# Kernel optimization log

Measured on AMD Instinct MI355X. Metric: run time of the kernel, lower is better.

Reference implementation:

```python
import jax, jax.numpy as jnp
import numpy as np

N = 10000      # nodes
ND = 64        # node_dim
H = 128        # hidden_dim
L = 4          # num_layers
K = 16         # knn k
TD = 16        # time_dim


def _time_embed(t, n):
    # sinusoidal embedding, matches _time_embed: freqs = exp(linspace(0,1,half)*-4)
    half = TD // 2
    freqs = jnp.exp(jnp.linspace(0.0, 1.0, half) * -4.0)            # [half]
    angles = t.reshape(1, 1) * freqs[None, :]                        # [1, half]
    emb = jnp.concatenate([jnp.sin(angles), jnp.cos(angles)], -1)    # [1, TD]
    return jnp.broadcast_to(emb, (n, TD))


def _knn_edges(pos, k):
    # full cdist + topk, mirroring _knn_graph (no_grad in torch)
    n = pos.shape[0]
    sq = jnp.sum(pos * pos, -1)
    d2 = sq[:, None] + sq[None, :] - 2.0 * (pos @ pos.T)             # [N, N]
    idxr = jnp.arange(n)
    d2 = d2.at[idxr, idxr].set(jnp.inf)
    _, nbr = jax.lax.top_k(-d2, k)                                   # [N, K] nearest
    src = jnp.repeat(idxr, k)
    dst = nbr.reshape(-1)
    return src, dst


def _egnn_layer(h, pos, src, dst, s, ew1, eb1, ew2, eb2, nw1, nb1, nw2, nb2, cw, cb):
    n = h.shape[0]
    diff = pos[dst] - pos[src]                                       # [E, 3]
    r2 = jnp.sum(diff * diff, -1, keepdims=True)                     # [E, 1]
    r = jnp.sqrt(r2 + 1e-8)
    dir_ij = diff / r
    e_in = jnp.concatenate([h[dst], h[src], r2], -1)                 # [E, 2H+1]
    m = jax.nn.silu(e_in @ ew1 + eb1)
    m = jax.nn.silu(m @ ew2 + eb2)                                   # [E, H]
    m = m * s[src][:, None]                                          # s-gate
    m_sum = jax.ops.segment_sum(m, dst, num_segments=n)              # [N, H]
    deg = jax.ops.segment_sum(jnp.ones((m.shape[0], 1), m.dtype), dst, num_segments=n)
    deg = jnp.maximum(deg, 1.0)
    m_sum = m_sum / deg
    hn = jax.nn.silu(jnp.concatenate([h, m_sum], -1) @ nw1 + nb1)
    h_new = hn @ nw2 + nb2                                           # [N, H]
    gamma = m @ cw + cb                                              # [E, 1]
    cu = jax.ops.segment_sum(gamma * dir_ij, dst, num_segments=n) / deg
    return h_new, pos + cu


def setup_inputs() -> dict:
    key = jax.random.key(0)
    ks = jax.random.split(key, 24)
    g = lambda k, shape: (jax.random.normal(k, shape, dtype=jnp.float32) * 0.05)
    z = lambda shape: jnp.zeros(shape, jnp.float32)
    return {
        'x': jax.random.normal(ks[0], (N, ND), jnp.float32),
        'pos': jax.random.normal(ks[1], (N, 3), jnp.float32) * 5.0,
        't': jax.random.uniform(ks[2], (1,), jnp.float32),
        's': jax.random.uniform(ks[3], (N,), jnp.float32),
        'proj_w': g(ks[4], (ND + 1 + TD, H)), 'proj_b': z((H,)),
        'edge_w1': g(ks[5], (L, 2 * H + 1, H)), 'edge_b1': z((L, H)),
        'edge_w2': g(ks[6], (L, H, H)), 'edge_b2': z((L, H)),
        'node_w1': g(ks[7], (L, 2 * H, H)), 'node_b1': z((L, H)),
        'node_w2': g(ks[8], (L, H, H)), 'node_b2': z((L, H)),
        'coord_w': g(ks[9], (L, H, 1)), 'coord_b': z((L, 1)),
        'ec_w': g(ks[10], (H, 3)), 'ec_b': z((3,)),
        'ef_w': g(ks[11], (H, ND)), 'ef_b': z((ND,)),
    }


def reference(x, pos, t, s, proj_w, proj_b, edge_w1, edge_b1, edge_w2, edge_b2,
              node_w1, node_b1, node_w2, node_b2, coord_w, coord_b,
              ec_w, ec_b, ef_w, ef_b):
    n = x.shape[0]
    src, dst = _knn_edges(jax.lax.stop_gradient(pos), K)  # graph build is no_grad
    temb = _time_embed(t[0], n)
    h = jnp.concatenate([x, s[:, None], temb], -1) @ proj_w + proj_b  # [N, H]
    p = pos
    for l in range(L):
        h, p = _egnn_layer(h, p, src, dst, s,
                           edge_w1[l], edge_b1[l], edge_w2[l], edge_b2[l],
                           node_w1[l], node_b1[l], node_w2[l], node_b2[l],
                           coord_w[l], coord_b[l])
    eps_c = h @ ec_w + ec_b                                           # [N, 3]
    eps_f = h @ ef_w + ef_b                                           # [N, ND]
    return jnp.concatenate([eps_c, eps_f, p], -1)                     # [N, 3+ND+3]
```

## Files before the change

### kernel.cpp

```cpp
#include <hip/hip_runtime.h>
#include <math.h>

#define N_NODES 10000
#define ND 64
#define H 128
#define LAYERS 4
#define KNN 16
#define TD 16
#define E_EDGES (N_NODES * KNN)
#define KC 1250
#define TILE_E 128
#define INF __builtin_inff()

typedef __attribute__((ext_vector_type(8))) short short8;
typedef __attribute__((ext_vector_type(4))) float f32x4;

__device__ __forceinline__ float silu(float x) {
  return x * __builtin_amdgcn_rcpf(1.0f + __expf(-x));
}

__device__ __forceinline__ unsigned short f2bf(float f) {
  unsigned int u = __float_as_uint(f);
  u += 0x7fffu + ((u >> 16) & 1u);
  return (unsigned short)(u >> 16);
}
__device__ __forceinline__ float bf2f(unsigned short h) {
  return __uint_as_float(((unsigned int)h) << 16);
}

__device__ __forceinline__ float dpp_shr1_f(float x) {
  return __int_as_float(__builtin_amdgcn_update_dpp(
      0, __float_as_int(x), 0x111, 0xF, 0xF, true));
}
__device__ __forceinline__ int dpp_shr1_i(int x) {
  return __builtin_amdgcn_update_dpp(0, x, 0x111, 0xF, 0xF, true);
}
__device__ __forceinline__ float rdlane_f(float x, int sl) {
  return __int_as_float(__builtin_amdgcn_readlane(__float_as_int(x), sl));
}

__global__ __launch_bounds__(256) void init_kernel(
    const float* __restrict__ ew2, const float* __restrict__ nw1,
    const float* __restrict__ nw2, const float* __restrict__ ew1,
    const float* __restrict__ pw, const float* __restrict__ ecw,
    const float* __restrict__ efw, unsigned short* __restrict__ w2T,
    unsigned short* __restrict__ nw1T, unsigned short* __restrict__ nw2T,
    unsigned short* __restrict__ ew1T, unsigned short* __restrict__ pwT,
    unsigned short* __restrict__ owT, const float* __restrict__ pos,
    float4* __restrict__ pos4, float* __restrict__ p0,
    int* __restrict__ degi) {
  int bid = blockIdx.x;
  if (bid < 1624) {
    int i = bid * 256 + threadIdx.x;
    if (i < 65536) {
      int l = i >> 14, rem = i & 16383, c = rem >> 7, o = rem & 127;
      w2T[l * 16384 + o * 128 + c] = f2bf(ew2[i]);
    } else if (i < 196608) {
      int j = i - 65536;
      int l = j >> 15, rem = j & 32767, c2 = rem >> 7, o = rem & 127;
      nw1T[l * 32768 + o * 256 + c2] = f2bf(nw1[j]);
    } else if (i < 262144) {
      int j = i - 196608;
      int l = j >> 14, rem = j & 16383, c = rem >> 7, o = rem & 127;
      nw2T[l * 16384 + o * 128 + c] = f2bf(nw2[j]);
    } else if (i < 393216) {
      int j = i - 262144;
      int l = j >> 15, rem = j & 32767, r = rem >> 7, o = rem & 127;
      int o2 = o + ((r >> 7) << 7);
      int c = r & 127;
      ew1T[l * 32768 + o2 * 128 + c] = f2bf(ew1[l * 257 * 128 + r * 128 + o]);
    } else if (i < 405504) {
      int j = i - 393216;
      int o = j / 96, c = j - o * 96;
      pwT[j] = (c < 81) ? f2bf(pw[c * 128 + o]) : 0;
    } else if (i < 415744) {
      int j = i - 405504;
      int o = j >> 7, c = j & 127;
      float v = 0.0f;
      if (o < 3) v = ecw[c * 3 + o];
      else if (o < 67) v = efw[c * 64 + (o - 3)];
      owT[j] = f2bf(v);
    }
  } else {
    int i = (bid - 1624) * 256 + threadIdx.x;
    if (i >= N_NODES) return;
    float x = pos[i * 3 + 0], y = pos[i * 3 + 1], z = pos[i * 3 + 2];
    pos4[i] = make_float4(x, y, z, x * x + y * y + z * z);
    p0[i * 3 + 0] = x;
    p0[i * 3 + 1] = y;
    p0[i * 3 + 2] = z;
    degi[i] = 0;
  }
}

#define DIST1(pp, d)                                                         \
  d = fmaf(ax, (pp).x, fmaf(ay, (pp).y, fmaf(az, (pp).z, (pp).w)));

#define GRP(dv, gbase)                                                       \
  {                                                                          \
    unsigned long long m = __ballot((dv) < th);                              \
    if (m) {                                                                 \
      while (m) {                                                            \
        int sl = __ffsll((long long)m) - 1;                                  \
        m &= m - 1;                                                          \
        float db = rdlane_f((dv), sl);                                       \
        int gj = (gbase) + sl;                                               \
        float pv = dpp_shr1_f(v);                                            \
        int pid = dpp_shr1_i(id);                                            \
        bool stay = (v <= db);                                               \
        bool tk = (lane == 0) || (pv <= db);                                 \
        v = stay ? v : (tk ? db : pv);                                       \
        id = stay ? id : (tk ? gj : pid);                                    \
      }                                                                      \
      th = rdlane_f(v, 15);                                                  \
    }                                                                        \
  }

#define SELF_FIX(j0base)                                                     \
  {                                                                          \
    unsigned rel = (unsigned)(q - (j0base));                                 \
    if (rel < 256u) {                                                        \
      int rl = (int)(rel & 63u);                                             \
      if (rel < 64u) { if (lane == rl) dA = INF; }                           \
      else if (rel < 128u) { if (lane == rl) dB = INF; }                     \
      else if (rel < 192u) { if (lane == rl) dC = INF; }                     \
      else { if (lane == rl) dD = INF; }                                     \
    }                                                                        \
  }

__global__ __launch_bounds__(256) void knn_kernel(const float4* __restrict__ pos4,
                                                  int* __restrict__ nbr,
                                                  int* __restrict__ degi) {
  __shared__ float4 C[KC];
  int tid = threadIdx.x;
  int lane = tid & 63;
  int wid = tid >> 6;
  int q = blockIdx.x * 4 + wid;
  float4 qp = pos4[q];
  float ax = -2.0f * qp.x, ay = -2.0f * qp.y, az = -2.0f * qp.z;
  float v = INF;
  int id = 0;
  float th = INF;
  for (int base = 0; base < N_NODES; base += KC) {
    __syncthreads();
    for (int jj = tid; jj < KC; jj += 256) C[jj] = pos4[base + jj];
    __syncthreads();
    for (int j0 = 0; j0 < 1024; j0 += 256) {
      float4 pA = C[j0 + lane], pB = C[j0 + 64 + lane];
      float4 pC = C[j0 + 128 + lane], pD = C[j0 + 192 + lane];
      float dA, dB, dC, dD;
      DIST1(pA, dA);
      DIST1(pB, dB);
      DIST1(pC, dC);
      DIST1(pD, dD);
      float mn = fminf(fminf(dA, dB), fminf(dC, dD));
      if (__ballot(mn < th)) {
        int gb = base + j0;
        SELF_FIX(gb);
        GRP(dA, gb);
        GRP(dB, gb + 64);
        GRP(dC, gb + 128);
        GRP(dD, gb + 192);
      }
    }
    {
      float4 pA = C[1024 + lane], pB = C[1088 + lane], pC = C[1152 + lane];
      float dA, dB, dC;
      float dD = INF;
      DIST1(pA, dA);
      DIST1(pB, dB);
      DIST1(pC, dC);
      if (lane < 34) {
        float4 pD = C[1216 + lane];
        DIST1(pD, dD);
      }
      float mn = fminf(fminf(dA, dB), fminf(dC, dD));
      if (__ballot(mn < th)) {
        int gb = base + 1024;
        SELF_FIX(gb);
        GRP(dA, gb);
        GRP(dB, gb + 64);
        GRP(dC, gb + 128);
        GRP(dD, gb + 192);
      }
    }
  }
  if (lane < KNN) {
    nbr[q * KNN + lane] = id;
    atomicAdd(&degi[id], 1);
  }
}

__global__ __launch_bounds__(1024) void scan_kernel(const int* __restrict__ degi,
                                                    int* __restrict__ off,
                                                    int* __restrict__ cursor) {
  __shared__ int part[1024];
  int t = threadIdx.x;
  int base = t * 10;
  int sum = 0;
  if (t < 1000)
    for (int i = 0; i < 10; ++i) sum += degi[base + i];
  part[t] = sum;
  __syncthreads();
  for (int stp = 1; stp < 1024; stp <<= 1) {
    int v = (t >= stp) ? part[t - stp] : 0;
    __syncthreads();
    part[t] += v;
    __syncthreads();
  }
  if (t < 1000) {
    int run = (t == 0) ? 0 : part[t - 1];
    for (int i = 0; i < 10; ++i) {
      off[base + i] = run;
      cursor[base + i] = run;
      run += degi[base + i];
    }
  }
  if (t == 0) off[N_NODES] = E_EDGES;
}

__global__ void scatter_kernel(const int* __restrict__ nbr, int* __restrict__ cursor,
                               int* __restrict__ eid, int* __restrict__ dstof) {
  int e = blockIdx.x * 256 + threadIdx.x;
  if (e < E_EDGES) {
    int d = nbr[e];
    int p = atomicAdd(&cursor[d], 1);
    eid[p] = e;
    dstof[p] = d;
  }
}

__global__ __launch_bounds__(256) void sort_proj_kernel(
    const float* __restrict__ x, const float* __restrict__ s,
    const float* __restrict__ tptr, const unsigned short* __restrict__ pwT,
    const float* __restrict__ pb, const unsigned short* __restrict__ ew1T,
    const float* __restrict__ eb1, float* __restrict__ h_out,
    unsigned short* __restrict__ Abf, unsigned short* __restrict__ Bbf,
    const int* __restrict__ off, int* __restrict__ eid) {
  __shared__ unsigned short inpb[16][104];
  __shared__ unsigned short hb[16][136];
  int tid = threadIdx.x;
  int bid = blockIdx.x;
  if (bid >= 625) {
    int n = (bid - 625) * 256 + tid;
    if (n >= N_NODES) return;
    int a = off[n], b = off[n + 1];
    for (int i = a + 1; i < b; ++i) {
      int v = eid[i];
      int j = i - 1;
      while (j >= a && eid[j] > v) { eid[j + 1] = eid[j]; --j; }
      eid[j + 1] = v;
    }
    return;
  }
  int n0 = bid * 16;
  float t = tptr[0];
  for (int idx = tid; idx < 16 * 104; idx += 256) {
    int n = idx / 104, c = idx - n * 104;
    int gn = n0 + n;
    float val;
    if (c < 64) val = x[gn * ND + c];
    else if (c == 64) val = s[gn];
    else if (c < 81) {
      int j = c - 65;
      int jj = (j < 8) ? j : (j - 8);
      float f = __expf(-4.0f * (float)jj / 7.0f);
      float a = t * f;
      val = (j < 8) ? sinf(a) : cosf(a);
    } else val = 0.0f;
    inpb[n][c] = f2bf(val);
  }
  __syncthreads();
  int w = tid >> 6, lane = tid & 63, fr = lane & 15, kg = lane >> 4;
  f32x4 acc[2];
  acc[0] = (f32x4){0.f, 0.f, 0.f, 0.f};
  acc[1] = (f32x4){0.f, 0.f, 0.f, 0.f};
#pragma unroll
  for (int ks = 0; ks < 3; ++ks) {
    int k = ks * 32 + kg * 8;
    short8 a = *(const short8*)&inpb[fr][k];
#pragma unroll
    for (int nt = 0; nt < 2; ++nt) {
      int col = w * 32 + nt * 16 + fr;
      short8 b = *(const short8*)&pwT[col * 96 + k];
      acc[nt] = __builtin_amdgcn_mfma_f32_16x16x32_bf16(a, b, acc[nt], 0, 0, 0);
    }
  }
#pragma unroll
  for (int nt = 0; nt < 2; ++nt) {
    int col = w * 32 + nt * 16 + fr;
    float bias = pb[col];
#pragma unroll
    for (int r = 0; r < 4; ++r) {
      int row = kg * 4 + r;
      float hv = acc[nt][r] + bias;
      h_out[(n0 + row) * H + col] = hv;
      hb[row][col] = f2bf(hv);
    }
  }
  __syncthreads();
  f32x4 acc2[4];
#pragma unroll
  for (int nt = 0; nt < 4; ++nt) acc2[nt] = (f32x4){0.f, 0.f, 0.f, 0.f};
#pragma unroll
  for (int ks = 0; ks < 4; ++ks) {
    int k = ks * 32 + kg * 8;
    short8 a = *(const short8*)&hb[fr][k];
#pragma unroll
    for (int nt = 0; nt < 4; ++nt) {
      int col = w * 64 + nt * 16 + fr;
      short8 b = *(const short8*)&ew1T[col * H + k];
      acc2[nt] = __builtin_amdgcn_mfma_f32_16x16x32_bf16(a, b, acc2[nt], 0, 0, 0);
    }
  }
#pragma unroll
  for (int nt = 0; nt < 4; ++nt) {
    int col = w * 64 + nt * 16 + fr;
    float bias = (col < H) ? eb1[col] : 0.0f;
#pragma unroll
    for (int r = 0; r < 4; ++r) {
      int row = kg * 4 + r;
      float val = acc2[nt][r] + bias;
      if (col < H) Abf[(n0 + row) * H + col] = f2bf(val);
      else Bbf[(n0 + row) * H + (col - H)] = f2bf(val);
    }
  }
}

__global__ __launch_bounds__(256) void edge_mfma_kernel(
    const unsigned short* __restrict__ Abf, const unsigned short* __restrict__ Bbf,
    const float* __restrict__ p, const float* __restrict__ s,
    const int* __restrict__ csr_off, const int* __restrict__ eid,
    const int* __restrict__ dstof, const float* __restrict__ wr,
    const unsigned short* __restrict__ w2T, const float* __restrict__ eb2,
    const float* __restrict__ cw, const float* __restrict__ cbp,
    float* __restrict__ msA, float* __restrict__ msB,
    float* __restrict__ cuA, float* __restrict__ cuB) {
  __shared__ unsigned short t1s[TILE_E][136];
  __shared__ float r2A[TILE_E], sA[TILE_E], dirA[TILE_E][3], gA[TILE_E];
  __shared__ int srcA[TILE_E], dstA[TILE_E];
  __shared__ float wrs[H], b2s[H], cws[H];

  int tid = threadIdx.x;
  int P0 = blockIdx.x * TILE_E;
  int P1 = P0 + TILE_E;

  if (tid < H) { wrs[tid] = wr[tid]; b2s[tid] = eb2[tid]; cws[tid] = cw[tid]; }
  if (tid < TILE_E) {
    int e = tid;
    int edge = eid[P0 + e];
    int src = edge >> 4;
    int d = dstof[P0 + e];
    srcA[e] = src;
    dstA[e] = d;
    float dx = p[d * 3 + 0] - p[src * 3 + 0];
    float dy = p[d * 3 + 1] - p[src * 3 + 1];
    float dz = p[d * 3 + 2] - p[src * 3 + 2];
    float r2 = dx * dx + dy * dy + dz * dz;
    r2A[e] = r2;
    float rinv = 1.0f / sqrtf(r2 + 1e-8f);
    dirA[e][0] = dx * rinv;
    dirA[e][1] = dy * rinv;
    dirA[e][2] = dz * rinv;
    sA[e] = s[src];
  }
  __syncthreads();

  int nA = dstA[0], nB = dstA[TILE_E - 1];
  int nn = nB - nA + 1;

  for (int idx = tid; idx < TILE_E * 16; idx += 256) {
    int e = idx >> 4, cp = (idx & 15) * 8;
    uint4 au = *(const uint4*)&Abf[dstA[e] * H + cp];
    uint4 bu = *(const uint4*)&Bbf[srcA[e] * H + cp];
    float r2v = r2A[e];
    unsigned int as[4] = {au.x, au.y, au.z, au.w};
    unsigned int bs[4] = {bu.x, bu.y, bu.z, bu.w};
    unsigned int res[4];
#pragma unroll
    for (int q = 0; q < 4; ++q) {
      float pr0 = silu(bf2f((unsigned short)(as[q] & 0xffffu)) +
                       bf2f((unsigned short)(bs[q] & 0xffffu)) +
                       r2v * wrs[cp + 2 * q]);
      float pr1 = silu(bf2f((unsigned short)(as[q] >> 16)) +
                       bf2f((unsigned short)(bs[q] >> 16)) +
                       r2v * wrs[cp + 2 * q + 1]);
      res[q] = ((unsigned int)f2bf(pr1) << 16) | (unsigned int)f2bf(pr0);
    }
    *(uint4*)&t1s[e][cp] = make_uint4(res[0], res[1], res[2], res[3]);
  }
  __syncthreads();

  int w = tid >> 6, lane = tid & 63;
  int fr = lane & 15, kg = lane >> 4;
  f32x4 acc[8][2];
#pragma unroll
  for (int mt = 0; mt < 8; ++mt)
#pragma unroll
    for (int nt = 0; nt < 2; ++nt) acc[mt][nt] = (f32x4){0.f, 0.f, 0.f, 0.f};
#pragma unroll
  for (int ks = 0; ks < 4; ++ks) {
    int k = ks * 32 + kg * 8;
    short8 bf0 = *(const short8*)&w2T[(w * 32 + fr) * H + k];
    short8 bf1 = *(const short8*)&w2T[(w * 32 + 16 + fr) * H + k];
#pragma unroll
    for (int mt = 0; mt < 8; ++mt) {
      short8 a = *(const short8*)&t1s[mt * 16 + fr][k];
      acc[mt][0] = __builtin_amdgcn_mfma_f32_16x16x32_bf16(a, bf0, acc[mt][0], 0, 0, 0);
      acc[mt][1] = __builtin_amdgcn_mfma_f32_16x16x32_bf16(a, bf1, acc[mt][1], 0, 0, 0);
    }
  }
  __syncthreads();

#pragma unroll
  for (int mt = 0; mt < 8; ++mt) {
#pragma unroll
    for (int nt = 0; nt < 2; ++nt) {
      int col = w * 32 + nt * 16 + fr;
      float b2v = b2s[col];
#pragma unroll
      for (int r = 0; r < 4; ++r) {
        int row = mt * 16 + kg * 4 + r;
        float mv = silu(acc[mt][nt][r] + b2v) * sA[row];
        t1s[row][col] = f2bf(mv);
      }
    }
  }
  __syncthreads();

  if (tid < TILE_E) {
    float g = 0.f;
    for (int c = 0; c < H; c += 4) {
      uint2 u = *(const uint2*)&t1s[tid][c];
      g = fmaf(bf2f((unsigned short)(u.x & 0xffffu)), cws[c], g);
      g = fmaf(bf2f((unsigned short)(u.x >> 16)), cws[c + 1], g);
      g = fmaf(bf2f((unsigned short)(u.y & 0xffffu)), cws[c + 2], g);
      g = fmaf(bf2f((unsigned short)(u.y >> 16)), cws[c + 3], g);
    }
    gA[tid] = g + cbp[0];
  }
  __syncthreads();

  for (int idx = tid; idx < nn * 32; idx += 256) {
    int ni = idx >> 5, cq = (idx & 31) * 4;
    int n = nA + ni;
    int o0 = csr_off[n], o1 = csr_off[n + 1];
    int lo = max(o0, P0), hi = min(o1, P1);
    float s0 = 0.f, s1 = 0.f, s2 = 0.f, s3 = 0.f;
    for (int pos = lo; pos < hi; ++pos) {
      uint2 u = *(const uint2*)&t1s[pos - P0][cq];
      s0 += bf2f((unsigned short)(u.x & 0xffffu));
      s1 += bf2f((unsigned short)(u.x >> 16));
      s2 += bf2f((unsigned short)(u.y & 0xffffu));
      s3 += bf2f((unsigned short)(u.y >> 16));
    }
    float4 sv = make_float4(s0, s1, s2, s3);
    if (o0 >= P0) {
      *(float4*)&msA[n * H + cq] = sv;
      if (o1 <= P1) *(float4*)&msB[n * H + cq] = make_float4(0.f, 0.f, 0.f, 0.f);
    } else {
      *(float4*)&msB[n * H + cq] = sv;
    }
  }
  for (int idx = tid; idx < nn * 3; idx += 256) {
    int ni = idx / 3, comp = idx - ni * 3;
    int n = nA + ni;
    int o0 = csr_off[n], o1 = csr_off[n + 1];
    int lo = max(o0, P0), hi = min(o1, P1);
    float sum = 0.f;
    for (int pos = lo; pos < hi; ++pos)
      sum += gA[pos - P0] * dirA[pos - P0][comp];
    if (o0 >= P0) {
      cuA[n * 3 + comp] = sum;
      if (o1 <= P1) cuB[n * 3 + comp] = 0.0f;
    } else {
      cuB[n * 3 + comp] = sum;
    }
  }
}

__global__ __launch_bounds__(256) void node_mfma_kernel(
    const float* __restrict__ h, const float* __restrict__ msA,
    const float* __restrict__ msB, const int* __restrict__ degi,
    const float* __restrict__ cuA, const float* __restrict__ cuB,
    const float* __restrict__ p_in, const unsigned short* __restrict__ w1T,
    const float* __restrict__ nb1, const unsigned short* __restrict__ w2T,
    const float* __restrict__ nb2, const unsigned short* __restrict__ ew1Tn,
    const float* __restrict__ eb1n, int doab, float* __restrict__ h_out,
    float* __restrict__ p_out, unsigned short* __restrict__ Abf,
    unsigned short* __restrict__ Bbf) {
  __shared__ unsigned short insb[16][264];
  __shared__ unsigned short hnsb[16][136];
  int tid = threadIdx.x;
  int n0 = blockIdx.x * 16;
  for (int idx = tid; idx < 16 * 32; idx += 256) {
    int n = idx >> 5, cq = (idx & 31) * 4;
    int gn = n0 + n;
    float4 hv = *(const float4*)&h[gn * H + cq];
    int dg = degi[gn];
    float m0 = 0.f, m1 = 0.f, m2 = 0.f, m3 = 0.f;
    if (dg > 0) {
      float4 a = *(const float4*)&msA[gn * H + cq];
      float4 b = *(const float4*)&msB[gn * H + cq];
      float fdg = (float)dg;
      m0 = (a.x + b.x) / fdg;
      m1 = (a.y + b.y) / fdg;
      m2 = (a.z + b.z) / fdg;
      m3 = (a.w + b.w) / fdg;
    }
    uint2 uh, um;
    uh.x = ((unsigned int)f2bf(hv.y) << 16) | (unsigned int)f2bf(hv.x);
    uh.y = ((unsigned int)f2bf(hv.w) << 16) | (unsigned int)f2bf(hv.z);
    um.x = ((unsigned int)f2bf(m1) << 16) | (unsigned int)f2bf(m0);
    um.y = ((unsigned int)f2bf(m3) << 16) | (unsigned int)f2bf(m2);
    *(uint2*)&insb[n][cq] = uh;
    *(uint2*)&insb[n][H + cq] = um;
  }
  __syncthreads();
  int w = tid >> 6, lane = tid & 63, fr = lane & 15, kg = lane >> 4;
  f32x4 acc[2];
  acc[0] = (f32x4){0.f, 0.f, 0.f, 0.f};
  acc[1] = (f32x4){0.f, 0.f, 0.f, 0.f};
#pragma unroll
  for (int ks = 0; ks < 8; ++ks) {
    int k = ks * 32 + kg * 8;
    short8 a = *(const short8*)&insb[fr][k];
#pragma unroll
    for (int nt = 0; nt < 2; ++nt) {
      int col = w * 32 + nt * 16 + fr;
      short8 b = *(const short8*)&w1T[col * 256 + k];
      acc[nt] = __builtin_amdgcn_mfma_f32_16x16x32_bf16(a, b, acc[nt], 0, 0, 0);
    }
  }
#pragma unroll
  for (int nt = 0; nt < 2; ++nt) {
    int col = w * 32 + nt * 16 + fr;
    float b1 = nb1[col];
#pragma unroll
    for (int r = 0; r < 4; ++r) {
      int row = kg * 4 + r;
      hnsb[row][col] = f2bf(silu(acc[nt][r] + b1));
    }
  }
  __syncthreads();
  f32x4 acc2[2];
  acc2[0] = (f32x4){0.f, 0.f, 0.f, 0.f};
  acc2[1] = (f32x4){0.f, 0.f, 0.f, 0.f};
#pragma unroll
  for (int ks = 0; ks < 4; ++ks) {
    int k = ks * 32 + kg * 8;
    short8 a = *(const short8*)&hnsb[fr][k];
#pragma unroll
    for (int nt = 0; nt < 2; ++nt) {
      int col = w * 32 + nt * 16 + fr;
      short8 b = *(const short8*)&w2T[col * H + k];
      acc2[nt] = __builtin_amdgcn_mfma_f32_16x16x32_bf16(a, b, acc2[nt], 0, 0, 0);
    }
  }
  unsigned short (*hb)[136] = (unsigned short(*)[136])insb;
#pragma unroll
  for (int nt = 0; nt < 2; ++nt) {
    int col = w * 32 + nt * 16 + fr;
    float b2 = nb2[col];
#pragma unroll
    for (int r = 0; r < 4; ++r) {
      int row = kg * 4 + r;
      float hv = acc2[nt][r] + b2;
      h_out[(n0 + row) * H + col] = hv;
      hb[row][col] = f2bf(hv);
    }
  }
  if (tid < 48) {
    int nl = tid / 3, comp = tid - nl * 3;
    int gn = n0 + nl;
    int dg = degi[gn];
    float add = 0.0f;
    if (dg > 0)
      add = (cuA[gn * 3 + comp] + cuB[gn * 3 + comp]) / (float)dg;
    p_out[gn * 3 + comp] = p_in[gn * 3 + comp] + add;
  }
  if (doab) {
    __syncthreads();
    f32x4 acc3[4];
#pragma unroll
    for (int nt = 0; nt < 4; ++nt) acc3[nt] = (f32x4){0.f, 0.f, 0.f, 0.f};
#pragma unroll
    for (int ks = 0; ks < 4; ++ks) {
      int k = ks * 32 + kg * 8;
      short8 a = *(const short8*)&hb[fr][k];
#pragma unroll
      for (int nt = 0; nt < 4; ++nt) {
        int col = w * 64 + nt * 16 + fr;
        short8 b = *(const short8*)&ew1Tn[col * H + k];
        acc3[nt] = __builtin_amdgcn_mfma_f32_16x16x32_bf16(a, b, acc3[nt], 0, 0, 0);
      }
    }
#pragma unroll
    for (int nt = 0; nt < 4; ++nt) {
      int col = w * 64 + nt * 16 + fr;
      float bias = (col < H) ? eb1n[col] : 0.0f;
#pragma unroll
      for (int r = 0; r < 4; ++r) {
        int row = kg * 4 + r;
        float val = acc3[nt][r] + bias;
        if (col < H) Abf[(n0 + row) * H + col] = f2bf(val);
        else Bbf[(n0 + row) * H + (col - H)] = f2bf(val);
      }
    }
  }
}

__global__ __launch_bounds__(256) void out_mfma_kernel(
    const float* __restrict__ h, const float* __restrict__ p,
    const unsigned short* __restrict__ owT, const float* __restrict__ ecb,
    const float* __restrict__ efb, float* __restrict__ out) {
  __shared__ unsigned short hb[16][136];
  int tid = threadIdx.x;
  int n0 = blockIdx.x * 16;
  for (int idx = tid; idx < 16 * H; idx += 256) {
    int n = idx >> 7, c = idx & 127;
    hb[n][c] = f2bf(h[(n0 + n) * H + c]);
  }
  __syncthreads();
  int w = tid >> 6, lane = tid & 63, fr = lane & 15, kg = lane >> 4;
  int ntiles = (w == 0) ? 2 : 1;
  for (int tt = 0; tt < ntiles; ++tt) {
    int tile = (tt == 0) ? w : 4;
    f32x4 acc = (f32x4){0.f, 0.f, 0.f, 0.f};
    int col = tile * 16 + fr;
#pragma unroll
    for (int ks = 0; ks < 4; ++ks) {
      int k = ks * 32 + kg * 8;
      short8 a = *(const short8*)&hb[fr][k];
      short8 b = *(const short8*)&owT[col * H + k];
      acc = __builtin_amdgcn_mfma_f32_16x16x32_bf16(a, b, acc, 0, 0, 0);
    }
    if (col < 67) {
      float bias = (col < 3) ? ecb[col] : efb[col - 3];
#pragma unroll
      for (int r = 0; r < 4; ++r) {
        int row = kg * 4 + r;
        out[(n0 + row) * 70 + col] = acc[r] + bias;
      }
    }
  }
  if (tid < 48) {
    int nl = tid / 3, comp = tid - nl * 3;
    int gn = n0 + nl;
    out[gn * 70 + 67 + comp] = p[gn * 3 + comp];
  }
}

extern "C" void kernel_launch(void* const* d_in, const int* in_sizes, int n_in,
                              void* d_out, int out_size, void* d_ws, size_t ws_size,
                              hipStream_t stream) {
  const float* x = (const float*)d_in[0];
  const float* pos = (const float*)d_in[1];
  const float* t = (const float*)d_in[2];
  const float* s = (const float*)d_in[3];
  const float* pw = (const float*)d_in[4];
  const float* pb = (const float*)d_in[5];
  const float* ew1 = (const float*)d_in[6];
  const float* eb1 = (const float*)d_in[7];
  const float* ew2 = (const float*)d_in[8];
  const float* eb2 = (const float*)d_in[9];
  const float* nw1 = (const float*)d_in[10];
  const float* nb1 = (const float*)d_in[11];
  const float* nw2 = (const float*)d_in[12];
  const float* nb2 = (const float*)d_in[13];
  const float* cw = (const float*)d_in[14];
  const float* cb = (const float*)d_in[15];
  const float* ecw = (const float*)d_in[16];
  const float* ecb = (const float*)d_in[17];
  const float* efw = (const float*)d_in[18];
  const float* efb = (const float*)d_in[19];

  char* wp = (char*)d_ws;
  auto alloc = [&](size_t bytes) {
    char* r = wp;
    wp += (bytes + 255) & ~(size_t)255;
    return r;
  };
  float* h0 = (float*)alloc((size_t)N_NODES * H * 4);
  float* h1 = (float*)alloc((size_t)N_NODES * H * 4);
  unsigned short* Abf = (unsigned short*)alloc((size_t)N_NODES * H * 2);
  unsigned short* Bbf = (unsigned short*)alloc((size_t)N_NODES * H * 2);
  float* msAb = (float*)alloc((size_t)N_NODES * H * 4);
  float* msBb = (float*)alloc((size_t)N_NODES * H * 4);
  float* cuAb = (float*)alloc((size_t)N_NODES * 3 * 4);
  float* cuBb = (float*)alloc((size_t)N_NODES * 3 * 4);
  float* p0 = (float*)alloc((size_t)N_NODES * 3 * 4);
  float* p1 = (float*)alloc((size_t)N_NODES * 3 * 4);
  int* degi = (int*)alloc((size_t)N_NODES * 4);
  int* nbr = (int*)alloc((size_t)E_EDGES * 4);
  int* off = (int*)alloc((size_t)(N_NODES + 1) * 4);
  int* cursor = (int*)alloc((size_t)N_NODES * 4);
  int* eid = (int*)alloc((size_t)E_EDGES * 4);
  int* dstof = (int*)alloc((size_t)E_EDGES * 4);
  unsigned short* w2Tb = (unsigned short*)alloc((size_t)LAYERS * H * H * 2);
  unsigned short* nw1Tb = (unsigned short*)alloc((size_t)LAYERS * 2 * H * H * 2);
  unsigned short* nw2Tb = (unsigned short*)alloc((size_t)LAYERS * H * H * 2);
  unsigned short* ew1Tb = (unsigned short*)alloc((size_t)LAYERS * 2 * H * H * 2);
  unsigned short* pwTb = (unsigned short*)alloc((size_t)H * 96 * 2);
  unsigned short* owTb = (unsigned short*)alloc((size_t)80 * H * 2);

  float4* pos4 = (float4*)msAb;

  init_kernel<<<1664, 256, 0, stream>>>(ew2, nw1, nw2, ew1, pw, ecw, efw,
                                        w2Tb, nw1Tb, nw2Tb, ew1Tb, pwTb, owTb,
                                        pos, pos4, p0, degi);
  knn_kernel<<<N_NODES / 4, 256, 0, stream>>>(pos4, nbr, degi);
  scan_kernel<<<1, 1024, 0, stream>>>(degi, off, cursor);
  scatter_kernel<<<(E_EDGES + 255) / 256, 256, 0, stream>>>(nbr, cursor, eid, dstof);
  sort_proj_kernel<<<665, 256, 0, stream>>>(x, s, t, pwTb, pb, ew1Tb, eb1,
                                            h0, Abf, Bbf, off, eid);

  float* hc = h0;
  float* hn = h1;
  float* pc = p0;
  float* pn = p1;
  for (int l = 0; l < LAYERS; ++l) {
    const float* ew1l = ew1 + (size_t)l * 257 * H;
    int doab = (l < LAYERS - 1) ? 1 : 0;
    edge_mfma_kernel<<<E_EDGES / TILE_E, 256, 0, stream>>>(
        Abf, Bbf, pc, s, off, eid, dstof, ew1l + 256 * H,
        w2Tb + (size_t)l * H * H, eb2 + l * H, cw + l * H, cb + l,
        msAb, msBb, cuAb, cuBb);
    node_mfma_kernel<<<N_NODES / 16, 256, 0, stream>>>(
        hc, msAb, msBb, degi, cuAb, cuBb, pc, nw1Tb + (size_t)l * 2 * H * H,
        nb1 + l * H, nw2Tb + (size_t)l * H * H, nb2 + l * H,
        ew1Tb + (size_t)(l + doab) * 2 * H * H, eb1 + (size_t)(l + doab) * H,
        doab, hn, pn, Abf, Bbf);
    float* tmp = hc; hc = hn; hn = tmp;
    tmp = pc; pc = pn; pn = tmp;
  }
  out_mfma_kernel<<<N_NODES / 16, 256, 0, stream>>>(hc, pc, owTb, ecb, efb,
                                                    (float*)d_out);
}
```

Baseline: 361.7 us.

## Replace brute-force kNN with uniform grid spatial hashing search

Replaces the all-pairs distance scan in the kNN kernel with a uniform 32^3 grid. A bounding box is computed with atomics, nodes are bucketed into cells via count/scan/scatter kernels, and each query searches expanding shells until the shell distance bound exceeds the current 16th-nearest distance. This removes the O(N^2) distance work but adds several small kernel launches, memsets, and irregular gathers of neighbor positions. Ties or boundary handling could order neighbors differently from the exact top_k.

Result: slower. 600.5 us (+66.0%).

```diff
diff --git a/kernel.cpp b/kernel.cpp
--- a/kernel.cpp
+++ b/kernel.cpp
@@ -8,8 +8,9 @@
 #define KNN 16
 #define TD 16
 #define E_EDGES (N_NODES * KNN)
-#define KC 1250
 #define TILE_E 128
+#define G 32
+#define NCELLS (G * G * G)
 #define INF __builtin_inff()
 
 typedef __attribute__((ext_vector_type(8))) short short8;
@@ -37,6 +38,31 @@
 }
 __device__ __forceinline__ float rdlane_f(float x, int sl) {
   return __int_as_float(__builtin_amdgcn_readlane(__float_as_int(x), sl));
+}
+
+__device__ __forceinline__ unsigned encf(float f) {
+  unsigned u = __float_as_uint(f);
+  return (u & 0x80000000u) ? ~u : (u | 0x80000000u);
+}
+__device__ __forceinline__ float decf(unsigned e) {
+  unsigned u = (e & 0x80000000u) ? (e & 0x7fffffffu) : ~e;
+  return __uint_as_float(u);
+}
+__device__ __forceinline__ void grid_params(const unsigned* __restrict__ bb,
+                                            float& mnx, float& mny, float& mnz,
+                                            float& cs) {
+  mnx = decf(bb[0]);
+  mny = decf(bb[1]);
+  mnz = decf(bb[2]);
+  float ex = decf(bb[3]) - mnx;
+  float ey = decf(bb[4]) - mny;
+  float ez = decf(bb[5]) - mnz;
+  float ext = fmaxf(ex, fmaxf(ey, ez));
+  cs = fmaxf(ext / (float)G, 1e-6f);
+}
+__device__ __forceinline__ int cellcoord(float x, float mn, float cs) {
+  int c = (int)floorf((x - mn) / cs);
+  return min(G - 1, max(0, c));
 }
 
 __global__ __launch_bounds__(256) void init_kernel(
@@ -48,7 +74,7 @@
     unsigned short* __restrict__ ew1T, unsigned short* __restrict__ pwT,
     unsigned short* __restrict__ owT, const float* __restrict__ pos,
     float4* __restrict__ pos4, float* __restrict__ p0,
-    int* __restrict__ degi) {
+    int* __restrict__ degi, unsigned* __restrict__ bbox) {
   int bid = blockIdx.x;
   if (bid < 1624) {
     int i = bid * 256 + threadIdx.x;
@@ -83,105 +109,167 @@
     }
   } else {
     int i = (bid - 1624) * 256 + threadIdx.x;
-    if (i >= N_NODES) return;
-    float x = pos[i * 3 + 0], y = pos[i * 3 + 1], z = pos[i * 3 + 2];
-    pos4[i] = make_float4(x, y, z, x * x + y * y + z * z);
-    p0[i * 3 + 0] = x;
-    p0[i * 3 + 1] = y;
-    p0[i * 3 + 2] = z;
-    degi[i] = 0;
-  }
+    bool ok = (i < N_NODES);
+    float x = 0.f, y = 0.f, z = 0.f;
+    if (ok) {
+      x = pos[i * 3 + 0];
+      y = pos[i * 3 + 1];
+      z = pos[i * 3 + 2];
+      pos4[i] = make_float4(x, y, z, x * x + y * y + z * z);
+      p0[i * 3 + 0] = x;
+      p0[i * 3 + 1] = y;
+      p0[i * 3 + 2] = z;
+      degi[i] = 0;
+    }
+    float mnx = ok ? x : INF, mny = ok ? y : INF, mnz = ok ? z : INF;
+    float mxx = ok ? x : -INF, mxy = ok ? y : -INF, mxz = ok ? z : -INF;
+    for (int o = 32; o > 0; o >>= 1) {
+      mnx = fminf(mnx, __shfl_xor(mnx, o, 64));
+      mny = fminf(mny, __shfl_xor(mny, o, 64));
+      mnz = fminf(mnz, __shfl_xor(mnz, o, 64));
+      mxx = fmaxf(mxx, __shfl_xor(mxx, o, 64));
+      mxy = fmaxf(mxy, __shfl_xor(mxy, o, 64));
+      mxz = fmaxf(mxz, __shfl_xor(mxz, o, 64));
+    }
+    if ((threadIdx.x & 63) == 0) {
+      atomicMin(&bbox[0], encf(mnx));
+      atomicMin(&bbox[1], encf(mny));
+      atomicMin(&bbox[2], encf(mnz));
+      atomicMax(&bbox[3], encf(mxx));
+      atomicMax(&bbox[4], encf(mxy));
+      atomicMax(&bbox[5], encf(mxz));
+    }
+  }
+}
+
+__global__ __launch_bounds__(256) void cell_kernel(const float* __restrict__ pos,
+                                                   const unsigned* __restrict__ bbox,
+                                                   int* __restrict__ cellof,
+                                                   int* __restrict__ cellcnt) {
+  int i = blockIdx.x * 256 + threadIdx.x;
+  if (i >= N_NODES) return;
+  float mnx, mny, mnz, cs;
+  grid_params(bbox, mnx, mny, mnz, cs);
+  int cx = cellcoord(pos[i * 3 + 0], mnx, cs);
+  int cy = cellcoord(pos[i * 3 + 1], mny, cs);
+  int cz = cellcoord(pos[i * 3 + 2], mnz, cs);
+  int cid = (cz * G + cy) * G + cx;
+  cellof[i] = cid;
+  atomicAdd(&cellcnt[cid], 1);
+}
+
+__global__ __launch_bounds__(1024) void cellscan_kernel(
+    const int* __restrict__ cellcnt, int* __restrict__ celloff,
+    int* __restrict__ cellcur) {
+  __shared__ int part[1024];
+  int t = threadIdx.x;
+  int base = t * 32;
+  int sum = 0;
+  for (int i = 0; i < 32; ++i) sum += cellcnt[base + i];
+  part[t] = sum;
+  __syncthreads();
+  for (int stp = 1; stp < 1024; stp <<= 1) {
+    int v = (t >= stp) ? part[t - stp] : 0;
+    __syncthreads();
+    part[t] += v;
+    __syncthreads();
+  }
+  int run = (t == 0) ? 0 : part[t - 1];
+  for (int i = 0; i < 32; ++i) {
+    celloff[base + i] = run;
+    cellcur[base + i] = run;
+    run += cellcnt[base + i];
+  }
+  if (t == 0) celloff[NCELLS] = N_NODES;
+}
+
+__global__ __launch_bounds__(256) void cellscatter_kernel(
+    const int* __restrict__ cellof, int* __restrict__ cellcur,
+    int* __restrict__ cellNodes) {
+  int i = blockIdx.x * 256 + threadIdx.x;
+  if (i >= N_NODES) return;
+  int p = atomicAdd(&cellcur[cellof[i]], 1);
+  cellNodes[p] = i;
 }
 
 #define DIST1(pp, d)                                                         \
   d = fmaf(ax, (pp).x, fmaf(ay, (pp).y, fmaf(az, (pp).z, (pp).w)));
 
-#define GRP(dv, gbase)                                                       \
+#define PROC_RUN(CY, CZ, X0, X1)                                             \
   {                                                                          \
-    unsigned long long m = __ballot((dv) < th);                              \
-    if (m) {                                                                 \
-      while (m) {                                                            \
-        int sl = __ffsll((long long)m) - 1;                                  \
-        m &= m - 1;                                                          \
-        float db = rdlane_f((dv), sl);                                       \
-        int gj = (gbase) + sl;                                               \
-        float pv = dpp_shr1_f(v);                                            \
-        int pid = dpp_shr1_i(id);                                            \
-        bool stay = (v <= db);                                               \
-        bool tk = (lane == 0) || (pv <= db);                                 \
-        v = stay ? v : (tk ? db : pv);                                       \
-        id = stay ? id : (tk ? gj : pid);                                    \
+    int cy_ = (CY), cz_ = (CZ);                                              \
+    if ((unsigned)cy_ < (unsigned)G && (unsigned)cz_ < (unsigned)G) {        \
+      int x0_ = max((X0), 0), x1_ = min((X1), G - 1);                        \
+      if (x0_ <= x1_) {                                                      \
+        int cb_ = (cz_ * G + cy_) * G;                                       \
+        int st_ = celloff[cb_ + x0_];                                        \
+        int en_ = celloff[cb_ + x1_ + 1];                                    \
+        for (int r0 = st_; r0 < en_; r0 += 64) {                             \
+          int ii = r0 + lane;                                                \
+          float d = INF;                                                     \
+          int cidx = 0;                                                      \
+          if (ii < en_) {                                                    \
+            cidx = cellNodes[ii];                                            \
+            float4 pp = pos4[cidx];                                          \
+            DIST1(pp, d);                                                    \
+            if (cidx == q) d = INF;                                          \
+          }                                                                  \
+          unsigned long long m = __ballot(d < th);                           \
+          if (m) {                                                           \
+            while (m) {                                                      \
+              int sl = __ffsll((long long)m) - 1;                            \
+              m &= m - 1;                                                    \
+              float db = rdlane_f(d, sl);                                    \
+              int gj = __builtin_amdgcn_readlane(cidx, sl);                  \
+              float pv = dpp_shr1_f(v);                                      \
+              int pid = dpp_shr1_i(id);                                      \
+              bool stay = (v <= db);                                         \
+              bool tk = (lane == 0) || (pv <= db);                           \
+              v = stay ? v : (tk ? db : pv);                                 \
+              id = stay ? id : (tk ? gj : pid);                              \
+            }                                                                \
+            th = rdlane_f(v, 15);                                            \
+          }                                                                  \
+        }                                                                    \
       }                                                                      \
-      th = rdlane_f(v, 15);                                                  \
     }                                                                        \
   }
 
-#define SELF_FIX(j0base)                                                     \
-  {                                                                          \
-    unsigned rel = (unsigned)(q - (j0base));                                 \
-    if (rel < 256u) {                                                        \
-      int rl = (int)(rel & 63u);                                             \
-      if (rel < 64u) { if (lane == rl) dA = INF; }                           \
-      else if (rel < 128u) { if (lane == rl) dB = INF; }                     \
-      else if (rel < 192u) { if (lane == rl) dC = INF; }                     \
-      else { if (lane == rl) dD = INF; }                                     \
-    }                                                                        \
-  }
-
-__global__ __launch_bounds__(256) void knn_kernel(const float4* __restrict__ pos4,
-                                                  int* __restrict__ nbr,
-                                                  int* __restrict__ degi) {
-  __shared__ float4 C[KC];
+__global__ __launch_bounds__(256) void knn_kernel(
+    const float4* __restrict__ pos4, const int* __restrict__ celloff,
+    const int* __restrict__ cellNodes, const unsigned* __restrict__ bbox,
+    int* __restrict__ nbr, int* __restrict__ degi) {
   int tid = threadIdx.x;
   int lane = tid & 63;
   int wid = tid >> 6;
   int q = blockIdx.x * 4 + wid;
   float4 qp = pos4[q];
   float ax = -2.0f * qp.x, ay = -2.0f * qp.y, az = -2.0f * qp.z;
+  float qw = qp.w;
+  float mnx, mny, mnz, cs;
+  grid_params(bbox, mnx, mny, mnz, cs);
+  int qcx = cellcoord(qp.x, mnx, cs);
+  int qcy = cellcoord(qp.y, mny, cs);
+  int qcz = cellcoord(qp.z, mnz, cs);
   float v = INF;
   int id = 0;
   float th = INF;
-  for (int base = 0; base < N_NODES; base += KC) {
-    __syncthreads();
-    for (int jj = tid; jj < KC; jj += 256) C[jj] = pos4[base + jj];
-    __syncthreads();
-    for (int j0 = 0; j0 < 1024; j0 += 256) {
-      float4 pA = C[j0 + lane], pB = C[j0 + 64 + lane];
-      float4 pC = C[j0 + 128 + lane], pD = C[j0 + 192 + lane];
-      float dA, dB, dC, dD;
-      DIST1(pA, dA);
-      DIST1(pB, dB);
-      DIST1(pC, dC);
-      DIST1(pD, dD);
-      float mn = fminf(fminf(dA, dB), fminf(dC, dD));
-      if (__ballot(mn < th)) {
-        int gb = base + j0;
-        SELF_FIX(gb);
-        GRP(dA, gb);
-        GRP(dB, gb + 64);
-        GRP(dC, gb + 128);
-        GRP(dD, gb + 192);
-      }
-    }
-    {
-      float4 pA = C[1024 + lane], pB = C[1088 + lane], pC = C[1152 + lane];
-      float dA, dB, dC;
-      float dD = INF;
-      DIST1(pA, dA);
-      DIST1(pB, dB);
-      DIST1(pC, dC);
-      if (lane < 34) {
-        float4 pD = C[1216 + lane];
-        DIST1(pD, dD);
-      }
-      float mn = fminf(fminf(dA, dB), fminf(dC, dD));
-      if (__ballot(mn < th)) {
-        int gb = base + 1024;
-        SELF_FIX(gb);
-        GRP(dA, gb);
-        GRP(dB, gb + 64);
-        GRP(dC, gb + 128);
-        GRP(dD, gb + 192);
+  PROC_RUN(qcy, qcz, qcx, qcx);
+  for (int rho = 1; rho < G; ++rho) {
+    if (th < INF) {
+      float bb = (float)(rho - 1) * cs;
+      if (bb * bb >= th + qw) break;
+    }
+    for (int dz = -rho; dz <= rho; ++dz) {
+      for (int dy = -rho; dy <= rho; ++dy) {
+        int ady = dy < 0 ? -dy : dy;
+        int adz = dz < 0 ? -dz : dz;
+        if (ady == rho || adz == rho) {
+          PROC_RUN(qcy + dy, qcz + dz, qcx - rho, qcx + rho);
+        } else {
+          PROC_RUN(qcy + dy, qcz + dz, qcx - rho, qcx - rho);
+          PROC_RUN(qcy + dy, qcz + dz, qcx + rho, qcx + rho);
+        }
       }
     }
   }
@@ -703,13 +791,27 @@
   unsigned short* ew1Tb = (unsigned short*)alloc((size_t)LAYERS * 2 * H * H * 2);
   unsigned short* pwTb = (unsigned short*)alloc((size_t)H * 96 * 2);
   unsigned short* owTb = (unsigned short*)alloc((size_t)80 * H * 2);
+  unsigned* bbox = (unsigned*)alloc(6 * 4);
+  int* cellof = (int*)alloc((size_t)N_NODES * 4);
+  int* cellcnt = (int*)alloc((size_t)NCELLS * 4);
+  int* celloff = (int*)alloc((size_t)(NCELLS + 1) * 4);
+  int* cellcur = (int*)alloc((size_t)NCELLS * 4);
+  int* cellNodes = (int*)alloc((size_t)N_NODES * 4);
 
   float4* pos4 = (float4*)msAb;
 
+  hipMemsetAsync(bbox, 0xFF, 12, stream);
+  hipMemsetAsync(bbox + 3, 0x00, 12, stream);
+  hipMemsetAsync(cellcnt, 0, (size_t)NCELLS * 4, stream);
   init_kernel<<<1664, 256, 0, stream>>>(ew2, nw1, nw2, ew1, pw, ecw, efw,
                                         w2Tb, nw1Tb, nw2Tb, ew1Tb, pwTb, owTb,
-                                        pos, pos4, p0, degi);
-  knn_kernel<<<N_NODES / 4, 256, 0, stream>>>(pos4, nbr, degi);
+                                        pos, pos4, p0, degi, bbox);
+  cell_kernel<<<(N_NODES + 255) / 256, 256, 0, stream>>>(pos, bbox, cellof, cellcnt);
+  cellscan_kernel<<<1, 1024, 0, stream>>>(cellcnt, celloff, cellcur);
+  cellscatter_kernel<<<(N_NODES + 255) / 256, 256, 0, stream>>>(cellof, cellcur,
+                                                                cellNodes);
+  knn_kernel<<<N_NODES / 4, 256, 0, stream>>>(pos4, celloff, cellNodes, bbox,
+                                              nbr, degi);
   scan_kernel<<<1, 1024, 0, stream>>>(degi, off, cursor);
   scatter_kernel<<<(E_EDGES + 255) / 256, 256, 0, stream>>>(nbr, cursor, eid, dstof);
   sort_proj_kernel<<<665, 256, 0, stream>>>(x, s, t, pwTb, pb, ew1Tb, eb1,
```
